# Performance work log

Measured on AMD Instinct MI355X. Metric: run time of the kernel, lower is better.

Reference implementation:

```python
import jax, jax.numpy as jnp
import numpy as np

ALPHA_FAST = 0.74
ALPHA_SLOW = 0.95
EPS = 1e-6


def setup_inputs() -> dict:
    key = jax.random.key(0)
    kA, kU = jax.random.split(key)
    A = jax.random.normal(kA, (8, 16, 64, 64, 64), dtype=jnp.float32)      # [B,M,T,H,W]
    U = jax.random.normal(kU, (8, 16, 2, 64, 64, 64), dtype=jnp.float32)   # [B,M,2,T,H,W]
    return {"A": A, "U": U}


def _ema_last(x, alpha):
    # Closed form of the causal EMA recurrence acc_t = a*acc_{t-1} + (1-a)*x_t,
    # evaluated only at the final timestep (the torch module discards all others):
    # acc_{T-1} = (1-a) * sum_t a^{T-1-t} x_t
    T = x.shape[2]
    t = jnp.arange(T)
    w = ((1.0 - alpha) * alpha ** (T - 1 - t)).astype(x.dtype)
    return jnp.einsum('bmthw,t->bmhw', x, w)


def _quad_energy_last(p):
    # p: [B,M,T,H,W]. quad_energy shifts by 2 frames (edge-replicated); at the
    # last frame: pq = 0.5*(p[T-1] - p[T-3])  (T >= 3).
    pq = 0.5 * (p[:, :, -1] - p[:, :, -3])
    return jnp.sqrt(jnp.maximum(p[:, :, -1] ** 2 + pq ** 2, EPS))


def reference(A, U):
    A_last = A[:, :, -1]                         # [B,M,H,W]
    A_fast = _ema_last(A, ALPHA_FAST)
    A_slow = _ema_last(A, ALPHA_SLOW)
    # torch.diff with prepend -> last element is A[T-1] - A[T-2]
    A_deriv = A[:, :, -1] - A[:, :, -2]
    E_re = _quad_energy_last(U[:, :, 0])
    E_im = _quad_energy_last(U[:, :, 1])
    E_temp = jnp.sqrt(jnp.maximum(E_re ** 2 + E_im ** 2, EPS))
    return jnp.concatenate([A_last, A_fast, A_slow, A_deriv, E_temp], axis=1)  # [B,5M,H,W]
```

## Files before the change

kernel.cpp:

```cpp
#include <hip/hip_runtime.h>
#include <math.h>

#define T_DIM 64
#define HW    4096
#define SPLITS 4

__device__ __forceinline__ void ema_step(float4& acc, const float4& x, float a, float oma) {
    acc.x = a * acc.x + oma * x.x;
    acc.y = a * acc.y + oma * x.y;
    acc.z = a * acc.z + oma * x.z;
    acc.w = a * acc.w + oma * x.w;
}

__global__ __launch_bounds__(256) void temporal_summarizer_kernel(
        const float* __restrict__ A, const float* __restrict__ U,
        float* __restrict__ out) {
    constexpr float AF = 0.74f, AS = 0.95f;
    constexpr float OMF = 1.0f - 0.74f, OMS = 1.0f - 0.95f;
    constexpr float EPS = 1e-6f;

    const int blk   = blockIdx.x;
    const int split = blk % SPLITS;
    const int bm    = blk / SPLITS;
    const int m     = bm & 15;
    const int b     = bm >> 4;

    const int pix = split * (HW / SPLITS) + threadIdx.x * 4;

    const float* pA = A + (size_t)bm * (T_DIM * HW) + pix;

    float4 fast = make_float4(0.f, 0.f, 0.f, 0.f);
    float4 slow = make_float4(0.f, 0.f, 0.f, 0.f);
    float4 a62  = make_float4(0.f, 0.f, 0.f, 0.f);
    float4 a63  = make_float4(0.f, 0.f, 0.f, 0.f);

    #pragma unroll 8
    for (int t = 0; t < T_DIM; ++t) {
        float4 x = *(const float4*)(pA + (size_t)t * HW);
        ema_step(fast, x, AF, OMF);
        ema_step(slow, x, AS, OMS);
        if (t == T_DIM - 2) a62 = x;
        if (t == T_DIM - 1) a63 = x;
    }

    const float* pU = U + (size_t)bm * (2 * T_DIM * HW) + pix;
    float4 u0l = *(const float4*)(pU + 63 * HW);
    float4 u0m = *(const float4*)(pU + 61 * HW);
    float4 u1l = *(const float4*)(pU + (size_t)T_DIM * HW + 63 * HW);
    float4 u1m = *(const float4*)(pU + (size_t)T_DIM * HW + 61 * HW);

    float4 et;
    {
        float* e = &et.x;
        const float* p0l = &u0l.x; const float* p0m = &u0m.x;
        const float* p1l = &u1l.x; const float* p1m = &u1m.x;
        #pragma unroll
        for (int i = 0; i < 4; ++i) {
            float pq0 = 0.5f * (p0l[i] - p0m[i]);
            float er  = sqrtf(fmaxf(p0l[i] * p0l[i] + pq0 * pq0, EPS));
            float pq1 = 0.5f * (p1l[i] - p1m[i]);
            float ei  = sqrtf(fmaxf(p1l[i] * p1l[i] + pq1 * pq1, EPS));
            e[i] = sqrtf(fmaxf(er * er + ei * ei, EPS));
        }
    }

    float4 deriv = make_float4(a63.x - a62.x, a63.y - a62.y,
                               a63.z - a62.z, a63.w - a62.w);

    float* ob = out + ((size_t)b * 80) * HW + (size_t)m * HW + pix;
    *(float4*)(ob + 0 * 16 * HW) = a63;
    *(float4*)(ob + 1 * 16 * HW) = fast;
    *(float4*)(ob + 2 * 16 * HW) = slow;
    *(float4*)(ob + 3 * 16 * HW) = deriv;
    *(float4*)(ob + 4 * 16 * HW) = et;
}

extern "C" void kernel_launch(void* const* d_in, const int* in_sizes, int n_in,
                              void* d_out, int out_size, void* d_ws, size_t ws_size,
                              hipStream_t stream) {
    const float* A = (const float*)d_in[0];
    const float* U = (const float*)d_in[1];
    float* out = (float*)d_out;
    dim3 grid(8 * 16 * SPLITS);
    dim3 block(256);
    temporal_summarizer_kernel<<<grid, block, 0, stream>>>(A, U, out);
}
```

Measured before the change: 373.7 us.

## Split temporal EMA across two time halves combined with atomic adds

```diff
diff --git a/kernel.cpp b/kernel.cpp
--- a/kernel.cpp
+++ b/kernel.cpp
@@ -1,78 +1,84 @@
 #include <hip/hip_runtime.h>
 #include <math.h>
 
+
 #define T_DIM 64
 #define HW    4096
-#define SPLITS 4
+#define HALF_T 32
 
-__device__ __forceinline__ void ema_step(float4& acc, const float4& x, float a, float oma) {
-    acc.x = a * acc.x + oma * x.x;
-    acc.y = a * acc.y + oma * x.y;
-    acc.z = a * acc.z + oma * x.z;
-    acc.w = a * acc.w + oma * x.w;
+typedef __attribute__((ext_vector_type(4))) float f4v;
+
+__device__ __forceinline__ f4v ntload4(const float* p) {
+    return __builtin_nontemporal_load((const f4v*)p);
 }
 
-__global__ __launch_bounds__(256) void temporal_summarizer_kernel(
+__global__ __launch_bounds__(256, 4) void temporal_summarizer_kernel(
         const float* __restrict__ A, const float* __restrict__ U,
-        float* __restrict__ out) {
+        float* __restrict__ out, float pf32, float ps32) {
     constexpr float AF = 0.74f, AS = 0.95f;
     constexpr float OMF = 1.0f - 0.74f, OMS = 1.0f - 0.95f;
     constexpr float EPS = 1e-6f;
 
     const int blk   = blockIdx.x;
-    const int split = blk % SPLITS;
-    const int bm    = blk / SPLITS;
+    const int hh    = blk & 1;
+    const int split = (blk >> 1) & 3;
+    const int bm    = blk >> 3;
     const int m     = bm & 15;
     const int b     = bm >> 4;
 
-    const int pix = split * (HW / SPLITS) + threadIdx.x * 4;
+    const int pix = split * (HW / 4) + threadIdx.x * 4;
 
-    const float* pA = A + (size_t)bm * (T_DIM * HW) + pix;
+    const float* pA = A + (size_t)bm * (T_DIM * HW) + (size_t)(hh * HALF_T) * HW + pix;
 
-    float4 fast = make_float4(0.f, 0.f, 0.f, 0.f);
-    float4 slow = make_float4(0.f, 0.f, 0.f, 0.f);
-    float4 a62  = make_float4(0.f, 0.f, 0.f, 0.f);
-    float4 a63  = make_float4(0.f, 0.f, 0.f, 0.f);
+    f4v fast = 0.f, slow = 0.f;
+    f4v a62 = 0.f, a63 = 0.f;
 
-    #pragma unroll 8
-    for (int t = 0; t < T_DIM; ++t) {
-        float4 x = *(const float4*)(pA + (size_t)t * HW);
-        ema_step(fast, x, AF, OMF);
-        ema_step(slow, x, AS, OMS);
-        if (t == T_DIM - 2) a62 = x;
-        if (t == T_DIM - 1) a63 = x;
+    #pragma unroll 16
+    for (int t = 0; t < HALF_T; ++t) {
+        f4v x = ntload4(pA + (size_t)t * HW);
+        fast = AF * fast + OMF * x;
+        slow = AS * slow + OMS * x;
+        if (hh && t == HALF_T - 2) a62 = x;
+        if (hh && t == HALF_T - 1) a63 = x;
     }
 
-    const float* pU = U + (size_t)bm * (2 * T_DIM * HW) + pix;
-    float4 u0l = *(const float4*)(pU + 63 * HW);
-    float4 u0m = *(const float4*)(pU + 61 * HW);
-    float4 u1l = *(const float4*)(pU + (size_t)T_DIM * HW + 63 * HW);
-    float4 u1m = *(const float4*)(pU + (size_t)T_DIM * HW + 61 * HW);
+    if (!hh) {
+        fast *= pf32;
+        slow *= ps32;
+    }
 
-    float4 et;
-    {
-        float* e = &et.x;
-        const float* p0l = &u0l.x; const float* p0m = &u0m.x;
-        const float* p1l = &u1l.x; const float* p1m = &u1m.x;
+    float* ofast = out + ((size_t)(b * 80 + 16 + m)) * HW + pix;
+    float* oslow = out + ((size_t)(b * 80 + 32 + m)) * HW + pix;
+    #pragma unroll
+    for (int i = 0; i < 4; ++i) {
+        atomicAdd(&ofast[i], fast[i]);
+        atomicAdd(&oslow[i], slow[i]);
+    }
+
+    if (hh) {
+        const float* pU = U + (size_t)bm * (2 * T_DIM * HW) + pix;
+        f4v u0l = ntload4(pU + 63 * HW);
+        f4v u0m = ntload4(pU + 61 * HW);
+        f4v u1l = ntload4(pU + (size_t)T_DIM * HW + 63 * HW);
+        f4v u1m = ntload4(pU + (size_t)T_DIM * HW + 61 * HW);
+
+        f4v et;
         #pragma unroll
         for (int i = 0; i < 4; ++i) {
-            float pq0 = 0.5f * (p0l[i] - p0m[i]);
-            float er  = sqrtf(fmaxf(p0l[i] * p0l[i] + pq0 * pq0, EPS));
-            float pq1 = 0.5f * (p1l[i] - p1m[i]);
-            float ei  = sqrtf(fmaxf(p1l[i] * p1l[i] + pq1 * pq1, EPS));
-            e[i] = sqrtf(fmaxf(er * er + ei * ei, EPS));
+            float pq0 = 0.5f * (u0l[i] - u0m[i]);
+            float er  = sqrtf(fmaxf(u0l[i] * u0l[i] + pq0 * pq0, EPS));
+            float pq1 = 0.5f * (u1l[i] - u1m[i]);
+            float ei  = sqrtf(fmaxf(u1l[i] * u1l[i] + pq1 * pq1, EPS));
+            et[i] = sqrtf(fmaxf(er * er + ei * ei, EPS));
         }
+
+        f4v deriv = a63 - a62;
+
+        float* ob = out + ((size_t)(b * 80 + m)) * HW + pix;
+        *(f4v*)(ob + 0 * 16 * HW) = a63;
+        *(f4v*)(ob + 48 * HW)     = deriv;
+        *(f4v*)(ob + 64 * HW)     = et;
     }
-
-    float4 deriv = make_float4(a63.x - a62.x, a63.y - a62.y,
-                               a63.z - a62.z, a63.w - a62.w);
-
-    float* ob = out + ((size_t)b * 80) * HW + (size_t)m * HW + pix;
-    *(float4*)(ob + 0 * 16 * HW) = a63;
-    *(float4*)(ob + 1 * 16 * HW) = fast;
-    *(float4*)(ob + 2 * 16 * HW) = slow;
-    *(float4*)(ob + 3 * 16 * HW) = deriv;
-    *(float4*)(ob + 4 * 16 * HW) = et;
 }
 
 extern "C" void kernel_launch(void* const* d_in, const int* in_sizes, int n_in,
@@ -81,7 +87,13 @@
     const float* A = (const float*)d_in[0];
     const float* U = (const float*)d_in[1];
     float* out = (float*)d_out;
-    dim3 grid(8 * 16 * SPLITS);
+
+    hipMemsetAsync(out, 0, (size_t)out_size * sizeof(float), stream);
+
+    const float pf32 = (float)pow(0.74, 32.0);
+    const float ps32 = (float)pow(0.95, 32.0);
+
+    dim3 grid(8 * 16 * 4 * 2);
     dim3 block(256);
-    temporal_summarizer_kernel<<<grid, block, 0, stream>>>(A, U, out);
+    temporal_summarizer_kernel<<<grid, block, 0, stream>>>(A, U, out, pf32, ps32);
 }
```

Result: slower. 390.2 us (+4.4%).
